# Kernel tuning notes

Hardware: AMD Instinct MI355X
Metric: run time of the kernel (lower is better)

## Reference

```python
import jax, jax.numpy as jnp
import numpy as np

N_HEADS = 16
D_HEAD = 64
IGNORE = -100000.0


def setup_inputs() -> dict:
    key = jax.random.key(0)
    ks = jax.random.split(key, 5)
    B, S, D = 2, 2048, 1024
    return {
        "residual": jax.random.normal(ks[0], (B, S, D), dtype=jnp.float32),
        "q": jax.random.normal(ks[1], (B, S, D), dtype=jnp.float32),
        "k": jax.random.normal(ks[2], (B, S, D), dtype=jnp.float32),
        "v": jax.random.normal(ks[3], (B, S, D), dtype=jnp.float32),
        "W_O": jax.random.normal(ks[4], (N_HEADS, D_HEAD, D), dtype=jnp.float32) * 0.02,
        "b_O": jnp.zeros((D,), dtype=jnp.float32),
    }


def reference(residual, q, k, v, W_O, b_O):
    B, S, _ = q.shape
    attn_scale = np.sqrt(D_HEAD).astype(np.float32)  # use_attn_scale=True
    # split heads: [..., pos, (h d)] -> [..., pos, h, d]
    qh = q.reshape(B, S, N_HEADS, D_HEAD)
    kh = k.reshape(B, S, N_HEADS, D_HEAD)
    vh = v.reshape(B, S, N_HEADS, D_HEAD)
    # scores: [..., head, query_pos, key_pos]
    scores = jnp.einsum("bqhd,bkhd->bhqk", qh, kh) / attn_scale
    causal = jnp.tril(jnp.ones((S, S), dtype=bool))
    scores = jnp.where(causal, scores, jnp.float32(IGNORE))
    pattern = jax.nn.softmax(scores, axis=-1)
    # weighted sum of values: [..., query_pos, head, d_head]
    z = jnp.einsum("bkhd,bhqk->bqhd", vh, pattern)
    out = jnp.einsum("bqhd,hdm->bqm", z, W_O) + b_O
    return (residual, out)
```

## Files before the change

kernel.cpp:

```cpp
#include <hip/hip_runtime.h>

#define B_ 2
#define S_ 2048
#define D_ 1024
#define H_ 16
#define DH_ 64
#define NP_ 2048

typedef short v8s __attribute__((ext_vector_type(8)));
typedef float v4f __attribute__((ext_vector_type(4)));
typedef float v16f __attribute__((ext_vector_type(16)));
typedef unsigned int v2u __attribute__((ext_vector_type(2)));
typedef unsigned int v4u __attribute__((ext_vector_type(4)));
typedef unsigned int uint32;

__device__ inline short f2bf(float f) {
  unsigned u = __float_as_uint(f);
  u = (u + 0x7FFFu + ((u >> 16) & 1u)) >> 16;
  return (short)u;
}

__device__ inline unsigned pk_bf16(float lo, float hi) {
  unsigned r;
  asm("v_cvt_pk_bf16_f32 %0, %1, %2" : "=v"(r) : "v"(lo), "v"(hi));
  return r;
}

__device__ inline void gll16(const void* g, void* l) {
  __builtin_amdgcn_global_load_lds(
      (const __attribute__((address_space(1))) void*)g,
      (__attribute__((address_space(3))) void*)l, 16, 0, 0);
}

__global__ __launch_bounds__(256) void cvt_all_kernel(
    const float* __restrict__ k, short* __restrict__ kb,
    const float* __restrict__ v, short* __restrict__ vt,
    const float* __restrict__ w, short* __restrict__ wt) {
  __shared__ short t[64][64 + 8];
  int bid = blockIdx.x;
  int tid = threadIdx.x;
  if (bid < 2048) {
    int i = bid * 256 + tid;
    float4 a = ((const float4*)k)[2 * i];
    float4 b = ((const float4*)k)[2 * i + 1];
    v8s o;
    o[0] = f2bf(a.x); o[1] = f2bf(a.y); o[2] = f2bf(a.z); o[3] = f2bf(a.w);
    o[4] = f2bf(b.x); o[5] = f2bf(b.y); o[6] = f2bf(b.z); o[7] = f2bf(b.w);
    ((v8s*)kb)[i] = o;
    return;
  }
  int r = tid >> 2, c16 = (tid & 3) * 16;
  if (bid < 3072) {
    int id = bid - 2048;
    int st = id & 31;
    int bh = id >> 5;
    int b = bh >> 4, h = bh & 15;
    const float* vp = v + ((size_t)(b * S_ + st * 64 + r)) * D_ + h * DH_ + c16;
    for (int i = 0; i < 16; i += 4) {
      float4 a = *(const float4*)(vp + i);
      t[r][c16 + i + 0] = f2bf(a.x);
      t[r][c16 + i + 1] = f2bf(a.y);
      t[r][c16 + i + 2] = f2bf(a.z);
      t[r][c16 + i + 3] = f2bf(a.w);
    }
    __syncthreads();
    short* op = vt + ((size_t)((b * H_ + h) * DH_ + r)) * S_ + st * 64 + c16;
    v8s o0, o1;
    for (int j = 0; j < 8; ++j) { o0[j] = t[c16 + j][r]; o1[j] = t[c16 + 8 + j][r]; }
    *(v8s*)op = o0;
    *(v8s*)(op + 8) = o1;
  } else {
    int id = bid - 3072;
    int tk = id & 15, tm = id >> 4;
    const float* wp = w + (size_t)(tk * 64 + r) * D_ + tm * 64 + c16;
    for (int i = 0; i < 16; i += 4) {
      float4 a = *(const float4*)(wp + i);
      t[r][c16 + i + 0] = f2bf(a.x);
      t[r][c16 + i + 1] = f2bf(a.y);
      t[r][c16 + i + 2] = f2bf(a.z);
      t[r][c16 + i + 3] = f2bf(a.w);
    }
    __syncthreads();
    short* op = wt + (size_t)(tm * 64 + r) * D_ + tk * 64 + c16;
    v8s o0, o1;
    for (int j = 0; j < 8; ++j) { o0[j] = t[c16 + j][r]; o1[j] = t[c16 + 8 + j][r]; }
    *(v8s*)op = o0;
    *(v8s*)(op + 8) = o1;
  }
}

template <int MAXSP>
__global__ __launch_bounds__(128, 4) void attn_kernel(
    const float* __restrict__ q, const short* __restrict__ kbf,
    const short* __restrict__ vtb, uint32* __restrict__ Opart,
    float* __restrict__ Lsum, const float* __restrict__ residual,
    float* __restrict__ res_out) {
  constexpr int NBLK = (MAXSP == 4) ? 2560 : 1536;
  int bid = blockIdx.x;
  int bh = bid & 31;
  int sidx = bid >> 5;
  int qt, sp;
  if constexpr (MAXSP == 4) {
    if (sidx < 32) { qt = 31 - (sidx >> 2); sp = sidx & 3; }
    else if (sidx < 56) { int t = sidx - 32; qt = 23 - t / 3; sp = t % 3; }
    else if (sidx < 72) { int t = sidx - 56; qt = 15 - ((t) >> 1); sp = t & 1; }
    else { qt = 7 - (sidx - 72); sp = 0; }
  } else {
    if (sidx < 32) { qt = 31 - (sidx >> 1); sp = sidx & 1; }
    else { qt = 15 - (sidx - 32); sp = 0; }
  }
  const int ns = qt / (32 / MAXSP) + 1;
  const int nt = qt + 1;
  const int t0 = sp * nt / ns;
  const int t1 = (sp + 1) * nt / ns - 1;
  int b = bh >> 4, h = bh & 15;

  int tid = threadIdx.x;
  int wave = tid >> 6, lane = tid & 63;
  int l31 = lane & 31, h32 = lane >> 5;

  __shared__ short Klds[64][64];
  __shared__ short Vlds[64][64];

  const int qrow0 = qt * 64 + wave * 32;
  const int lr8 = lane >> 3;
  const int scol = ((lane & 7) ^ lr8) << 3;

  const short* kbase = kbf + (size_t)b * S_ * D_ + h * DH_ +
                       (size_t)(wave * 8 + lr8) * D_ + scol;
  const short* vbase = vtb + (size_t)(b * H_ + h) * DH_ * S_ +
                       (size_t)(wave * 8 + lr8) * S_ + scol;

  v8s qf[4];
  {
    const float* qp = q + (size_t)(b * S_ + qrow0 + l31) * D_ + h * DH_ + h32 * 8;
    const float sc = 0.125f * 1.44269504f;
#pragma unroll
    for (int d4 = 0; d4 < 4; ++d4) {
      float4 x = *(const float4*)(qp + d4 * 16);
      float4 y = *(const float4*)(qp + d4 * 16 + 4);
      v8s tq;
      tq[0] = f2bf(x.x * sc); tq[1] = f2bf(x.y * sc);
      tq[2] = f2bf(x.z * sc); tq[3] = f2bf(x.w * sc);
      tq[4] = f2bf(y.x * sc); tq[5] = f2bf(y.y * sc);
      tq[6] = f2bf(y.z * sc); tq[7] = f2bf(y.w * sc);
      qf[d4] = tq;
    }
  }

  v16f O0, O1;
#pragma unroll
  for (int r = 0; r < 16; ++r) { O0[r] = 0.f; O1[r] = 0.f; }
  float L = 0.f;
  const int swz = (l31 & 7) << 3;

  for (int s = t0; s <= t1; ++s) {
    {
      const short* kp = kbase + (size_t)(s * 64) * D_;
      const short* vp = vbase + s * 64;
#pragma unroll
      for (int i = 0; i < 4; ++i)
        gll16(kp + (size_t)(i * 16) * D_, &Klds[i * 16 + wave * 8][0]);
#pragma unroll
      for (int i = 0; i < 4; ++i)
        gll16(vp + (size_t)(i * 16) * S_, &Vlds[i * 16 + wave * 8][0]);
    }
    asm volatile("s_waitcnt vmcnt(0)" ::: "memory");
    __builtin_amdgcn_sched_barrier(0);
    __builtin_amdgcn_s_barrier();
    __builtin_amdgcn_sched_barrier(0);

    int kb = s * 64;
    bool skip1 = (kb >= qrow0);
    bool msk = (kb + 63 > qrow0);

    __builtin_amdgcn_s_setprio(1);
    v16f S0, S1;
#pragma unroll
    for (int r = 0; r < 16; ++r) { S0[r] = 0.f; S1[r] = 0.f; }
#pragma unroll
    for (int d4 = 0; d4 < 4; ++d4) {
      v8s kf = *(const v8s*)&Klds[l31][(((d4 << 1) | h32) << 3) ^ swz];
      S0 = __builtin_amdgcn_mfma_f32_32x32x16_bf16(kf, qf[d4], S0, 0, 0, 0);
    }
    if (!skip1) {
#pragma unroll
      for (int d4 = 0; d4 < 4; ++d4) {
        v8s kf = *(const v8s*)&Klds[32 + l31][(((d4 << 1) | h32) << 3) ^ swz];
        S1 = __builtin_amdgcn_mfma_f32_32x32x16_bf16(kf, qf[d4], S1, 0, 0, 0);
      }
    }
    __builtin_amdgcn_s_setprio(0);

    int qg = qrow0 + l31;
    if (msk) {
#pragma unroll
      for (int r = 0; r < 16; ++r) {
        int kl = kb + (r & 3) + 8 * (r >> 2) + 4 * h32;
        if (kl > qg) S0[r] = -1e30f;
      }
      if (!skip1) {
#pragma unroll
        for (int r = 0; r < 16; ++r) {
          int kl = kb + 32 + (r & 3) + 8 * (r >> 2) + 4 * h32;
          if (kl > qg) S1[r] = -1e30f;
        }
      }
    }

    float rs = 0.f;
    unsigned pw0[8], pw1[8];
#pragma unroll
    for (int r = 0; r < 16; ++r) {
      S0[r] = __builtin_amdgcn_exp2f(S0[r]);
      rs += S0[r];
    }
#pragma unroll
    for (int w = 0; w < 8; ++w) pw0[w] = pk_bf16(S0[2 * w], S0[2 * w + 1]);
    if (!skip1) {
#pragma unroll
      for (int r = 0; r < 16; ++r) {
        S1[r] = __builtin_amdgcn_exp2f(S1[r]);
        rs += S1[r];
      }
#pragma unroll
      for (int w = 0; w < 8; ++w) pw1[w] = pk_bf16(S1[2 * w], S1[2 * w + 1]);
    }
    rs += __shfl_xor(rs, 32);
    L += rs;

    __builtin_amdgcn_s_setprio(1);
#pragma unroll
    for (int ks = 0; ks < 2; ++ks) {
      v2u a = __builtin_amdgcn_permlane32_swap(pw0[ks * 4 + 0], pw0[ks * 4 + 2], false, false);
      v2u c = __builtin_amdgcn_permlane32_swap(pw0[ks * 4 + 1], pw0[ks * 4 + 3], false, false);
      v4u fw; fw.x = a.x; fw.y = c.x; fw.z = a.y; fw.w = c.y;
      v8s pb = __builtin_bit_cast(v8s, fw);
      v8s vf0 = *(const v8s*)&Vlds[l31][(((ks << 1) | h32) << 3) ^ swz];
      O0 = __builtin_amdgcn_mfma_f32_32x32x16_bf16(vf0, pb, O0, 0, 0, 0);
      v8s vf1 = *(const v8s*)&Vlds[32 + l31][(((ks << 1) | h32) << 3) ^ swz];
      O1 = __builtin_amdgcn_mfma_f32_32x32x16_bf16(vf1, pb, O1, 0, 0, 0);
    }
    if (!skip1) {
#pragma unroll
      for (int ks = 0; ks < 2; ++ks) {
        v2u a = __builtin_amdgcn_permlane32_swap(pw1[ks * 4 + 0], pw1[ks * 4 + 2], false, false);
        v2u c = __builtin_amdgcn_permlane32_swap(pw1[ks * 4 + 1], pw1[ks * 4 + 3], false, false);
        v4u fw; fw.x = a.x; fw.y = c.x; fw.z = a.y; fw.w = c.y;
        v8s pb = __builtin_bit_cast(v8s, fw);
        v8s vf0 = *(const v8s*)&Vlds[l31][((((ks + 2) << 1) | h32) << 3) ^ swz];
        O0 = __builtin_amdgcn_mfma_f32_32x32x16_bf16(vf0, pb, O0, 0, 0, 0);
        v8s vf1 = *(const v8s*)&Vlds[32 + l31][((((ks + 2) << 1) | h32) << 3) ^ swz];
        O1 = __builtin_amdgcn_mfma_f32_32x32x16_bf16(vf1, pb, O1, 0, 0, 0);
      }
    }
    __builtin_amdgcn_s_setprio(0);

    __builtin_amdgcn_sched_barrier(0);
    __builtin_amdgcn_s_barrier();
    __builtin_amdgcn_sched_barrier(0);
  }

  int p = bh * 64 + qt * 2 + wave;
  uint32* Op = Opart + ((size_t)(sp * NP_ + p)) * 1024;
#pragma unroll
  for (int w = 0; w < 8; ++w) {
    int dpair = 4 * (w >> 1) + (w & 1) + 2 * h32;
    Op[dpair * 32 + l31] = pk_bf16(O0[2 * w], O0[2 * w + 1]);
    Op[(16 + dpair) * 32 + l31] = pk_bf16(O1[2 * w], O1[2 * w + 1]);
  }
  if (h32 == 0) Lsum[(size_t)(sp * NP_ + p) * 32 + l31] = L;

  {
    const float4* rs_ = (const float4*)residual;
    float4* rd_ = (float4*)res_out;
    const int total = NBLK * 128;
    for (size_t i = (size_t)bid * 128 + tid; i < 1048576; i += total)
      rd_[i] = rs_[i];
  }
}

template <int MAXSP>
__global__ __launch_bounds__(128) void merge_kernel(
    const uint32* __restrict__ Opart, const float* __restrict__ Lsum,
    short* __restrict__ z) {
  int p = blockIdx.x;
  int qt = (p >> 1) & 31;
  const int ns = qt / (32 / MAXSP) + 1;
  int tid = threadIdx.x;
  int qq = tid & 31, g = tid >> 5;

  float Lt = 0.f;
#pragma unroll
  for (int sp = 0; sp < MAXSP; ++sp)
    if (sp < ns) Lt += Lsum[((size_t)sp * NP_ + p) * 32 + qq];
  float f = 1.f / Lt;

  __shared__ uint32 T[32][33];
#pragma unroll
  for (int j = 0; j < 8; ++j) {
    int dp = g * 8 + j;
    float lo = 0.f, hi = 0.f;
#pragma unroll
    for (int sp = 0; sp < MAXSP; ++sp)
      if (sp < ns) {
        uint32 u = Opart[((size_t)sp * NP_ + p) * 1024 + dp * 32 + qq];
        lo += __uint_as_float(u << 16);
        hi += __uint_as_float(u & 0xFFFF0000u);
      }
    T[qq][dp] = pk_bf16(lo * f, hi * f);
  }
  __syncthreads();
  int q2 = tid >> 2, c = (tid & 3) * 8;
  int srow = (p & 63) * 32 + q2;
  int b = p >> 10, h = (p >> 6) & 15;
  uint32* zp = (uint32*)z + ((size_t)(b * S_ + srow)) * (D_ / 2) + h * 32 + c;
#pragma unroll
  for (int j = 0; j < 8; ++j) zp[j] = T[q2][c + j];
}

__global__ __launch_bounds__(256) void proj_kernel(
    const short* __restrict__ z, const short* __restrict__ wt,
    const float* __restrict__ bias, float* __restrict__ out) {
  int bm = blockIdx.x, bn = blockIdx.y;
  int tid = threadIdx.x;
  int wave = tid >> 6, lane = tid & 63, lh = lane >> 4, ll = lane & 15;
  int wr = wave >> 1, wc = wave & 1;

  __shared__ short Al[2][64][64];
  __shared__ short Bl[2][128][64];

  const int r8 = lane >> 3;
  const int scol = ((lane & 7) ^ r8) << 3;

  v4f acc[2][4];
#pragma unroll
  for (int m = 0; m < 2; ++m)
#pragma unroll
    for (int n = 0; n < 4; ++n) acc[m][n] = (v4f){0.f, 0.f, 0.f, 0.f};

  auto stage = [&](int kb, int bbuf) {
#pragma unroll
    for (int i = 0; i < 2; ++i) {
      int c = wave * 2 + i;
      gll16(z + (size_t)(bm * 64 + c * 8 + r8) * D_ + kb + scol, &Al[bbuf][c * 8][0]);
    }
#pragma unroll
    for (int i = 0; i < 4; ++i) {
      int c = wave * 4 + i;
      gll16(wt + (size_t)(bn * 128 + c * 8 + r8) * D_ + kb + scol, &Bl[bbuf][c * 8][0]);
    }
  };

  stage(0, 0);
  __syncthreads();

  for (int kt = 0; kt < D_ / 64; ++kt) {
    int bbuf = kt & 1;
    if (kt + 1 < D_ / 64) stage((kt + 1) * 64, bbuf ^ 1);
    v8s af[2][2], bf[4][2];
#pragma unroll
    for (int m = 0; m < 2; ++m) {
      int row = wr * 32 + m * 16 + ll;
#pragma unroll
      for (int c = 0; c < 2; ++c)
        af[m][c] = *(const v8s*)&Al[bbuf][row][(((c << 2) | lh) ^ (ll & 7)) << 3];
    }
#pragma unroll
    for (int n = 0; n < 4; ++n) {
      int row = wc * 64 + n * 16 + ll;
#pragma unroll
      for (int c = 0; c < 2; ++c)
        bf[n][c] = *(const v8s*)&Bl[bbuf][row][(((c << 2) | lh) ^ (ll & 7)) << 3];
    }
#pragma unroll
    for (int m = 0; m < 2; ++m)
#pragma unroll
      for (int n = 0; n < 4; ++n)
#pragma unroll
        for (int c = 0; c < 2; ++c)
          acc[m][n] = __builtin_amdgcn_mfma_f32_16x16x32_bf16(af[m][c], bf[n][c], acc[m][n], 0, 0, 0);
    __syncthreads();
  }

#pragma unroll
  for (int m = 0; m < 2; ++m) {
    int gr = bm * 64 + wr * 32 + m * 16 + lh * 4;
#pragma unroll
    for (int n = 0; n < 4; ++n) {
      int gc = bn * 128 + wc * 64 + n * 16 + ll;
      float bo = bias[gc];
#pragma unroll
      for (int r = 0; r < 4; ++r)
        out[(size_t)(gr + r) * D_ + gc] = acc[m][n][r] + bo;
    }
  }
}

extern "C" void kernel_launch(void* const* d_in, const int* in_sizes, int n_in,
                              void* d_out, int out_size, void* d_ws, size_t ws_size,
                              hipStream_t stream) {
  const float* residual = (const float*)d_in[0];
  const float* q = (const float*)d_in[1];
  const float* k = (const float*)d_in[2];
  const float* v = (const float*)d_in[3];
  const float* W = (const float*)d_in[4];
  const float* bO = (const float*)d_in[5];
  float* out = (float*)d_out;

  const size_t half = (size_t)B_ * S_ * D_;
  char* ws = (char*)d_ws;
  short* kbf = (short*)ws;
  short* vtb = kbf + half;
  short* wtb = vtb + half;
  char* pbase = (char*)(wtb + (size_t)D_ * D_);
  const size_t opart_b = (size_t)NP_ * 1024 * 4;
  const size_t l_b = (size_t)NP_ * 32 * 4;
  const size_t base_b = (size_t)pbase - (size_t)ws;
  short* z = kbf;

  cvt_all_kernel<<<3328, 256, 0, stream>>>(k, kbf, v, vtb, W, wtb);

  if (ws_size >= base_b + 4 * (opart_b + l_b)) {
    uint32* Opart = (uint32*)pbase;
    float* Lsum = (float*)(pbase + 4 * opart_b);
    attn_kernel<4><<<2560, 128, 0, stream>>>(q, kbf, vtb, Opart, Lsum, residual, out);
    merge_kernel<4><<<NP_, 128, 0, stream>>>(Opart, Lsum, z);
    proj_kernel<<<dim3((B_ * S_) / 64, D_ / 128), 256, 0, stream>>>(z, wtb, bO, out + half);
  } else {
    uint32* Opart = (uint32*)pbase;
    float* Lsum = (float*)(pbase + 2 * opart_b);
    attn_kernel<2><<<1536, 128, 0, stream>>>(q, kbf, vtb, Opart, Lsum, residual, out);
    merge_kernel<2><<<NP_, 128, 0, stream>>>(Opart, Lsum, z);
    proj_kernel<<<dim3((B_ * S_) / 64, D_ / 128), 256, 0, stream>>>(z, wtb, bO, out + half);
  }
}
```

Measured before the change: 81.76 us.

## Double-buffer 32-key K/V tiles and use uniform 2-way split-K scheduling

The attention kernel now walks keys in 32-row tiles held in a double-buffered LDS ring, issuing the next tile's global-to-LDS loads before computing on the current one. The old uneven 1-4 split of key ranges per query tile is replaced by an even 2-way split (or none) with a snake ordering of query tiles, and fully masked tiles are skipped. This aims to hide load latency and cut the partial-merge traffic, at the cost of more loop iterations and barriers plus coarser load balancing for long causal rows.

```diff
diff --git a/kernel.cpp b/kernel.cpp
--- a/kernel.cpp
+++ b/kernel.cpp
@@ -89,47 +89,46 @@
   }
 }
 
-template <int MAXSP>
+template <int SPLITS>
 __global__ __launch_bounds__(128, 4) void attn_kernel(
     const float* __restrict__ q, const short* __restrict__ kbf,
     const short* __restrict__ vtb, uint32* __restrict__ Opart,
     float* __restrict__ Lsum, const float* __restrict__ residual,
     float* __restrict__ res_out) {
-  constexpr int NBLK = (MAXSP == 4) ? 2560 : 1536;
   int bid = blockIdx.x;
   int bh = bid & 31;
-  int sidx = bid >> 5;
-  int qt, sp;
-  if constexpr (MAXSP == 4) {
-    if (sidx < 32) { qt = 31 - (sidx >> 2); sp = sidx & 3; }
-    else if (sidx < 56) { int t = sidx - 32; qt = 23 - t / 3; sp = t % 3; }
-    else if (sidx < 72) { int t = sidx - 56; qt = 15 - ((t) >> 1); sp = t & 1; }
-    else { qt = 7 - (sidx - 72); sp = 0; }
+  int sp, qt;
+  if constexpr (SPLITS == 2) {
+    sp = (bid >> 5) & 1;
+    int g = (bid >> 6) & 3, j = bid >> 8;
+    qt = 31 - 4 * j - ((j & 1) ? 3 - g : g);
   } else {
-    if (sidx < 32) { qt = 31 - (sidx >> 1); sp = sidx & 1; }
-    else { qt = 15 - (sidx - 32); sp = 0; }
-  }
-  const int ns = qt / (32 / MAXSP) + 1;
-  const int nt = qt + 1;
-  const int t0 = sp * nt / ns;
-  const int t1 = (sp + 1) * nt / ns - 1;
+    sp = 0;
+    int g = (bid >> 5) & 3, j = bid >> 7;
+    qt = 31 - 4 * j - ((j & 1) ? 3 - g : g);
+  }
   int b = bh >> 4, h = bh & 15;
+
+  const int tt0 = (SPLITS == 2) ? sp * (qt + 1) : 0;
+  const int tt1 = (SPLITS == 2) ? tt0 + qt : 2 * qt + 1;
 
   int tid = threadIdx.x;
   int wave = tid >> 6, lane = tid & 63;
   int l31 = lane & 31, h32 = lane >> 5;
 
-  __shared__ short Klds[64][64];
-  __shared__ short Vlds[64][64];
+  __shared__ short Klds[2][32][64];
+  __shared__ short Vlds[2][32][64];
 
   const int qrow0 = qt * 64 + wave * 32;
   const int lr8 = lane >> 3;
-  const int scol = ((lane & 7) ^ lr8) << 3;
+  const int l7 = lane & 7;
 
   const short* kbase = kbf + (size_t)b * S_ * D_ + h * DH_ +
-                       (size_t)(wave * 8 + lr8) * D_ + scol;
+                       (size_t)(wave * 8 + lr8) * D_ + ((l7 ^ lr8) << 3);
+  const int vq = l7 ^ lr8;
   const short* vbase = vtb + (size_t)(b * H_ + h) * DH_ * S_ +
-                       (size_t)(wave * 8 + lr8) * S_ + scol;
+                       (size_t)(wave * 8 + lr8 + (vq >> 2) * 32) * S_ +
+                       ((vq & 3) << 3);
 
   v8s qf[4];
   {
@@ -154,107 +153,82 @@
   float L = 0.f;
   const int swz = (l31 & 7) << 3;
 
-  for (int s = t0; s <= t1; ++s) {
-    {
-      const short* kp = kbase + (size_t)(s * 64) * D_;
-      const short* vp = vbase + s * 64;
-#pragma unroll
-      for (int i = 0; i < 4; ++i)
-        gll16(kp + (size_t)(i * 16) * D_, &Klds[i * 16 + wave * 8][0]);
-#pragma unroll
-      for (int i = 0; i < 4; ++i)
-        gll16(vp + (size_t)(i * 16) * S_, &Vlds[i * 16 + wave * 8][0]);
-    }
-    asm volatile("s_waitcnt vmcnt(0)" ::: "memory");
+  auto stage = [&](int t, int buf) {
+    const short* kp = kbase + (size_t)(t * 32) * D_;
+    const short* vp = vbase + t * 32;
+#pragma unroll
+    for (int i = 0; i < 2; ++i)
+      gll16(kp + (size_t)(i * 16) * D_, &Klds[buf][i * 16 + wave * 8][0]);
+#pragma unroll
+    for (int i = 0; i < 2; ++i)
+      gll16(vp + (size_t)(i * 16) * S_, &Vlds[buf][i * 16 + wave * 8][0]);
+  };
+
+  stage(tt0, tt0 & 1);
+
+  for (int s = tt0; s <= tt1; ++s) {
+    int cur = s & 1;
+    if (s < tt1) {
+      stage(s + 1, cur ^ 1);
+      asm volatile("s_waitcnt vmcnt(4)" ::: "memory");
+    } else {
+      asm volatile("s_waitcnt vmcnt(0)" ::: "memory");
+    }
     __builtin_amdgcn_sched_barrier(0);
     __builtin_amdgcn_s_barrier();
     __builtin_amdgcn_sched_barrier(0);
 
-    int kb = s * 64;
-    bool skip1 = (kb >= qrow0);
-    bool msk = (kb + 63 > qrow0);
-
-    __builtin_amdgcn_s_setprio(1);
-    v16f S0, S1;
-#pragma unroll
-    for (int r = 0; r < 16; ++r) { S0[r] = 0.f; S1[r] = 0.f; }
-#pragma unroll
-    for (int d4 = 0; d4 < 4; ++d4) {
-      v8s kf = *(const v8s*)&Klds[l31][(((d4 << 1) | h32) << 3) ^ swz];
-      S0 = __builtin_amdgcn_mfma_f32_32x32x16_bf16(kf, qf[d4], S0, 0, 0, 0);
-    }
-    if (!skip1) {
+    int kb = s * 32;
+    bool fullskip = (kb > qrow0 + 31);
+    if (!fullskip) {
+      bool msk = (kb + 31 > qrow0);
+
+      __builtin_amdgcn_s_setprio(1);
+      v16f S0;
+#pragma unroll
+      for (int r = 0; r < 16; ++r) S0[r] = 0.f;
 #pragma unroll
       for (int d4 = 0; d4 < 4; ++d4) {
-        v8s kf = *(const v8s*)&Klds[32 + l31][(((d4 << 1) | h32) << 3) ^ swz];
-        S1 = __builtin_amdgcn_mfma_f32_32x32x16_bf16(kf, qf[d4], S1, 0, 0, 0);
+        v8s kf = *(const v8s*)&Klds[cur][l31][(((d4 << 1) | h32) << 3) ^ swz];
+        S0 = __builtin_amdgcn_mfma_f32_32x32x16_bf16(kf, qf[d4], S0, 0, 0, 0);
       }
-    }
-    __builtin_amdgcn_s_setprio(0);
-
-    int qg = qrow0 + l31;
-    if (msk) {
-#pragma unroll
-      for (int r = 0; r < 16; ++r) {
-        int kl = kb + (r & 3) + 8 * (r >> 2) + 4 * h32;
-        if (kl > qg) S0[r] = -1e30f;
-      }
-      if (!skip1) {
+      __builtin_amdgcn_s_setprio(0);
+
+      int qg = qrow0 + l31;
+      if (msk) {
 #pragma unroll
         for (int r = 0; r < 16; ++r) {
-          int kl = kb + 32 + (r & 3) + 8 * (r >> 2) + 4 * h32;
-          if (kl > qg) S1[r] = -1e30f;
+          int kl = kb + (r & 3) + 8 * (r >> 2) + 4 * h32;
+          if (kl > qg) S0[r] = -1e30f;
         }
       }
-    }
-
-    float rs = 0.f;
-    unsigned pw0[8], pw1[8];
-#pragma unroll
-    for (int r = 0; r < 16; ++r) {
-      S0[r] = __builtin_amdgcn_exp2f(S0[r]);
-      rs += S0[r];
-    }
-#pragma unroll
-    for (int w = 0; w < 8; ++w) pw0[w] = pk_bf16(S0[2 * w], S0[2 * w + 1]);
-    if (!skip1) {
+
+      float rs = 0.f;
+      unsigned pw0[8];
 #pragma unroll
       for (int r = 0; r < 16; ++r) {
-        S1[r] = __builtin_amdgcn_exp2f(S1[r]);
-        rs += S1[r];
+        S0[r] = __builtin_amdgcn_exp2f(S0[r]);
+        rs += S0[r];
       }
 #pragma unroll
-      for (int w = 0; w < 8; ++w) pw1[w] = pk_bf16(S1[2 * w], S1[2 * w + 1]);
-    }
-    rs += __shfl_xor(rs, 32);
-    L += rs;
-
-    __builtin_amdgcn_s_setprio(1);
-#pragma unroll
-    for (int ks = 0; ks < 2; ++ks) {
-      v2u a = __builtin_amdgcn_permlane32_swap(pw0[ks * 4 + 0], pw0[ks * 4 + 2], false, false);
-      v2u c = __builtin_amdgcn_permlane32_swap(pw0[ks * 4 + 1], pw0[ks * 4 + 3], false, false);
-      v4u fw; fw.x = a.x; fw.y = c.x; fw.z = a.y; fw.w = c.y;
-      v8s pb = __builtin_bit_cast(v8s, fw);
-      v8s vf0 = *(const v8s*)&Vlds[l31][(((ks << 1) | h32) << 3) ^ swz];
-      O0 = __builtin_amdgcn_mfma_f32_32x32x16_bf16(vf0, pb, O0, 0, 0, 0);
-      v8s vf1 = *(const v8s*)&Vlds[32 + l31][(((ks << 1) | h32) << 3) ^ swz];
-      O1 = __builtin_amdgcn_mfma_f32_32x32x16_bf16(vf1, pb, O1, 0, 0, 0);
-    }
-    if (!skip1) {
+      for (int w = 0; w < 8; ++w) pw0[w] = pk_bf16(S0[2 * w], S0[2 * w + 1]);
+      rs += __shfl_xor(rs, 32);
+      L += rs;
+
+      __builtin_amdgcn_s_setprio(1);
 #pragma unroll
       for (int ks = 0; ks < 2; ++ks) {
-        v2u a = __builtin_amdgcn_permlane32_swap(pw1[ks * 4 + 0], pw1[ks * 4 + 2], false, false);
-        v2u c = __builtin_amdgcn_permlane32_swap(pw1[ks * 4 + 1], pw1[ks * 4 + 3], false, false);
+        v2u a = __builtin_amdgcn_permlane32_swap(pw0[ks * 4 + 0], pw0[ks * 4 + 2], false, false);
+        v2u c = __builtin_amdgcn_permlane32_swap(pw0[ks * 4 + 1], pw0[ks * 4 + 3], false, false);
         v4u fw; fw.x = a.x; fw.y = c.x; fw.z = a.y; fw.w = c.y;
         v8s pb = __builtin_bit_cast(v8s, fw);
-        v8s vf0 = *(const v8s*)&Vlds[l31][((((ks + 2) << 1) | h32) << 3) ^ swz];
+        v8s vf0 = *(const v8s*)&Vlds[cur][l31][(((ks << 1) | h32) << 3) ^ swz];
         O0 = __builtin_amdgcn_mfma_f32_32x32x16_bf16(vf0, pb, O0, 0, 0, 0);
-        v8s vf1 = *(const v8s*)&Vlds[32 + l31][((((ks + 2) << 1) | h32) << 3) ^ swz];
+        v8s vf1 = *(const v8s*)&Vlds[cur][l31][(((4 | (ks << 1) | h32)) << 3) ^ swz];
         O1 = __builtin_amdgcn_mfma_f32_32x32x16_bf16(vf1, pb, O1, 0, 0, 0);
       }
-    }
-    __builtin_amdgcn_s_setprio(0);
+      __builtin_amdgcn_s_setprio(0);
+    }
 
     __builtin_amdgcn_sched_barrier(0);
     __builtin_amdgcn_s_barrier();
@@ -272,42 +246,38 @@
   if (h32 == 0) Lsum[(size_t)(sp * NP_ + p) * 32 + l31] = L;
 
   {
+    constexpr int NBLK = (SPLITS == 2) ? 2048 : 1024;
     const float4* rs_ = (const float4*)residual;
     float4* rd_ = (float4*)res_out;
-    const int total = NBLK * 128;
-    for (size_t i = (size_t)bid * 128 + tid; i < 1048576; i += total)
+    for (size_t i = (size_t)bid * 128 + tid; i < 1048576; i += (size_t)NBLK * 128)
       rd_[i] = rs_[i];
   }
 }
 
-template <int MAXSP>
+template <int SPLITS>
 __global__ __launch_bounds__(128) void merge_kernel(
     const uint32* __restrict__ Opart, const float* __restrict__ Lsum,
     short* __restrict__ z) {
   int p = blockIdx.x;
-  int qt = (p >> 1) & 31;
-  const int ns = qt / (32 / MAXSP) + 1;
   int tid = threadIdx.x;
   int qq = tid & 31, g = tid >> 5;
 
-  float Lt = 0.f;
-#pragma unroll
-  for (int sp = 0; sp < MAXSP; ++sp)
-    if (sp < ns) Lt += Lsum[((size_t)sp * NP_ + p) * 32 + qq];
+  float Lt = Lsum[(size_t)p * 32 + qq];
+  if constexpr (SPLITS == 2) Lt += Lsum[((size_t)NP_ + p) * 32 + qq];
   float f = 1.f / Lt;
 
   __shared__ uint32 T[32][33];
 #pragma unroll
   for (int j = 0; j < 8; ++j) {
     int dp = g * 8 + j;
-    float lo = 0.f, hi = 0.f;
-#pragma unroll
-    for (int sp = 0; sp < MAXSP; ++sp)
-      if (sp < ns) {
-        uint32 u = Opart[((size_t)sp * NP_ + p) * 1024 + dp * 32 + qq];
-        lo += __uint_as_float(u << 16);
-        hi += __uint_as_float(u & 0xFFFF0000u);
-      }
+    uint32 u0 = Opart[(size_t)p * 1024 + dp * 32 + qq];
+    float lo = __uint_as_float(u0 << 16);
+    float hi = __uint_as_float(u0 & 0xFFFF0000u);
+    if constexpr (SPLITS == 2) {
+      uint32 u1 = Opart[((size_t)NP_ + p) * 1024 + dp * 32 + qq];
+      lo += __uint_as_float(u1 << 16);
+      hi += __uint_as_float(u1 & 0xFFFF0000u);
+    }
     T[qq][dp] = pk_bf16(lo * f, hi * f);
   }
   __syncthreads();
@@ -421,17 +391,17 @@
 
   cvt_all_kernel<<<3328, 256, 0, stream>>>(k, kbf, v, vtb, W, wtb);
 
-  if (ws_size >= base_b + 4 * (opart_b + l_b)) {
+  if (ws_size >= base_b + 2 * (opart_b + l_b)) {
     uint32* Opart = (uint32*)pbase;
-    float* Lsum = (float*)(pbase + 4 * opart_b);
-    attn_kernel<4><<<2560, 128, 0, stream>>>(q, kbf, vtb, Opart, Lsum, residual, out);
-    merge_kernel<4><<<NP_, 128, 0, stream>>>(Opart, Lsum, z);
+    float* Lsum = (float*)(pbase + 2 * opart_b);
+    attn_kernel<2><<<2048, 128, 0, stream>>>(q, kbf, vtb, Opart, Lsum, residual, out);
+    merge_kernel<2><<<NP_, 128, 0, stream>>>(Opart, Lsum, z);
     proj_kernel<<<dim3((B_ * S_) / 64, D_ / 128), 256, 0, stream>>>(z, wtb, bO, out + half);
   } else {
     uint32* Opart = (uint32*)pbase;
-    float* Lsum = (float*)(pbase + 2 * opart_b);
-    attn_kernel<2><<<1536, 128, 0, stream>>>(q, kbf, vtb, Opart, Lsum, residual, out);
-    merge_kernel<2><<<NP_, 128, 0, stream>>>(Opart, Lsum, z);
+    float* Lsum = (float*)(pbase + opart_b);
+    attn_kernel<1><<<1024, 128, 0, stream>>>(q, kbf, vtb, Opart, Lsum, residual, out);
+    merge_kernel<1><<<NP_, 128, 0, stream>>>(Opart, Lsum, z);
     proj_kernel<<<dim3((B_ * S_) / 64, D_ / 128), 256, 0, stream>>>(z, wtb, bO, out + half);
   }
 }
```

Result: faster. 76.59 us (-6.3%).
